# Kernel tuning notes

Measured on AMD Instinct MI355X. Metric: run time of the kernel, lower is better.

Reference implementation:

```python
import jax, jax.numpy as jnp
import numpy as np
from jax import lax
import math

N_QUBITS = 10
N_LAYERS = 4
PI = jnp.float32(math.pi)


def _c(x):
    return x.astype(jnp.complex64)


def rx_mat(t):
    c = _c(jnp.cos(0.5 * t)); s = _c(jnp.sin(0.5 * t))
    return jnp.stack([jnp.stack([c, -1j * s]), jnp.stack([-1j * s, c])])


def ry_mat(t):
    c = _c(jnp.cos(0.5 * t)); s = _c(jnp.sin(0.5 * t))
    return jnp.stack([jnp.stack([c, -s]), jnp.stack([s, c])])


def rz_mat(t):
    e0 = jnp.exp(_c(jnp.zeros_like(t)) - 0.5j * _c(t))
    e1 = jnp.exp(0.5j * _c(t))
    z = jnp.zeros_like(e0)
    return jnp.stack([jnp.stack([e0, z]), jnp.stack([z, e1])])


def apply_1q(psi, U, q):
    # psi: (2,)*n complex, apply 2x2 U on axis q
    psi = jnp.moveaxis(psi, q, 0)
    psi = jnp.tensordot(U, psi, axes=(1, 0))
    return jnp.moveaxis(psi, 0, q)


def apply_cnot(psi, ctrl, tgt):
    psi = jnp.moveaxis(psi, (ctrl, tgt), (0, 1))
    a00, a01, a10, a11 = psi[0, 0], psi[0, 1], psi[1, 0], psi[1, 1]
    psi = jnp.stack([jnp.stack([a00, a01]), jnp.stack([a11, a10])])
    return jnp.moveaxis(psi, (0, 1), (ctrl, tgt))


def vqc(state, weights):
    # state: (D,) float32 angles; weights: (layers, n, 3)
    n, L = N_QUBITS, N_LAYERS
    D = state.shape[0]
    psi = jnp.full((2,) * n, 2.0 ** (-n / 2.0), dtype=jnp.complex64)  # H^n |0>
    for layer in range(L):
        for q in range(n):
            ang = state[(layer * n + q) % D]
            psi = apply_1q(psi, rx_mat(ang), q)
            psi = apply_1q(psi, ry_mat(ang), q)
            psi = apply_1q(psi, rz_mat(weights[layer, q, 0]), q)
            psi = apply_1q(psi, ry_mat(weights[layer, q, 1]), q)
            psi = apply_1q(psi, rz_mat(weights[layer, q, 2]), q)
        for q in range(n - 1):
            psi = apply_cnot(psi, q, q + 1)
        psi = apply_cnot(psi, n - 1, 0)
    probs = jnp.real(psi * jnp.conj(psi))  # (2,)*n
    zdiag = jnp.array([1.0, -1.0], dtype=jnp.float32)
    exps = [jnp.sum(probs * zdiag.reshape((1,) * q + (2,) + (1,) * (n - q - 1)))
            for q in range(n)]
    return jnp.stack(exps)  # (n,)


def lstm_forward(x, W_ih, W_hh, b_ih, b_hh):
    # x: [B,T,Din]; PyTorch gate order: i, f, g, o
    B, T, _ = x.shape
    H = W_hh.shape[1]
    b = b_ih + b_hh

    def step(carry, xt):
        h, c = carry
        gates = xt @ W_ih.T + h @ W_hh.T + b
        i, f, g, o = jnp.split(gates, 4, axis=-1)
        i = jax.nn.sigmoid(i); f = jax.nn.sigmoid(f)
        g = jnp.tanh(g); o = jax.nn.sigmoid(o)
        c = f * c + i * g
        h = o * jnp.tanh(c)
        return (h, c), h

    h0 = jnp.zeros((B, H), x.dtype)
    c0 = jnp.zeros((B, H), x.dtype)
    _, hs = lax.scan(step, (h0, c0), jnp.swapaxes(x, 0, 1))
    return jnp.swapaxes(hs, 0, 1)  # [B,T,H]


def _forward(s, lstm_s, W_ih, W_hh, b_ih, b_hh, proj_W, proj_b,
             in_proj_W, in_proj_b, out_proj_W, out_proj_b,
             qweights, W1, b1, W2, b2):
    hs = lstm_forward(lstm_s, W_ih, W_hh, b_ih, b_hh)      # [B,T,H]
    lstm_last = hs[:, -1, :]                               # [B,H]
    state_full = jnp.concatenate([lstm_last, s], axis=1)   # [B,E]
    lstm_proj = hs @ proj_W.T + proj_b                     # [B,T,E]
    E = proj_W.shape[0]
    Wq, Wk, Wv = in_proj_W[:E], in_proj_W[E:2 * E], in_proj_W[2 * E:]
    bq, bk, bv = in_proj_b[:E], in_proj_b[E:2 * E], in_proj_b[2 * E:]
    q = state_full @ Wq.T + bq                             # [B,E] (1 query token)
    k = lstm_proj @ Wk.T + bk                              # [B,T,E]
    v = lstm_proj @ Wv.T + bv
    scale = 1.0 / jnp.sqrt(jnp.float32(E))                 # num_heads=1 -> head_dim=E
    attn = jax.nn.softmax(jnp.einsum('be,bte->bt', q, k) * scale, axis=-1)
    ctx = jnp.einsum('bt,bte->be', attn, v)
    attn_out = ctx @ out_proj_W.T + out_proj_b             # [B,E]
    merged_state = jnp.concatenate([attn_out, s], axis=1)  # [B,E+F]
    state_norm = jnp.tanh(merged_state) * PI
    qfeat = jax.vmap(lambda st: vqc(st, qweights))(state_norm)  # [B,n]
    merged = jnp.concatenate([merged_state, qfeat], axis=1)
    x = jax.nn.relu(merged @ W1.T + b1)
    return x @ W2.T + b2


def setup_inputs() -> dict:
    key = jax.random.key(0)
    ks = jax.random.split(key, 16)
    B, T = 512, 256
    Din, H, F = 128, 256, 64
    E = H + F          # 320 = state_dim
    Dm = E + F         # 384 = merged_state dim
    n_l1, n_act = 512, 8

    def g(k, shape, std):
        return (std * jax.random.normal(k, shape)).astype(jnp.float32)

    return {
        's': jax.random.normal(ks[0], (B, F), jnp.float32),
        'lstm_s': jax.random.normal(ks[1], (B, T, Din), jnp.float32),
        'W_ih': g(ks[2], (4 * H, Din), 0.05),
        'W_hh': g(ks[3], (4 * H, H), 0.05),
        'b_ih': jnp.zeros((4 * H,), jnp.float32),
        'b_hh': jnp.zeros((4 * H,), jnp.float32),
        'proj_W': g(ks[4], (E, H), 0.05),
        'proj_b': 0.1 * jnp.ones((E,), jnp.float32),
        'in_proj_W': g(ks[5], (3 * E, E), 0.05),
        'in_proj_b': jnp.zeros((3 * E,), jnp.float32),
        'out_proj_W': g(ks[6], (E, E), 0.05),
        'out_proj_b': jnp.zeros((E,), jnp.float32),
        'qweights': jax.random.uniform(ks[7], (N_LAYERS, N_QUBITS, 3), jnp.float32, 0.0, 2.0 * math.pi),
        'W1': g(ks[8], (n_l1, Dm + N_QUBITS), 0.05),
        'b1': 0.1 * jnp.ones((n_l1,), jnp.float32),
        'W2': g(ks[9], (n_act, n_l1), 0.05),
        'b2': 0.1 * jnp.ones((n_act,), jnp.float32),
    }


def reference(s, lstm_s, W_ih, W_hh, b_ih, b_hh, proj_W, proj_b,
              in_proj_W, in_proj_b, out_proj_W, out_proj_b,
              qweights, W1, b1, W2, b2):
    return _forward(s, lstm_s, W_ih, W_hh, b_ih, b_hh, proj_W, proj_b,
                    in_proj_W, in_proj_b, out_proj_W, out_proj_b,
                    qweights, W1, b1, W2, b2)
```

## Files before the change

kernel.cpp:

```cpp
#include <hip/hip_runtime.h>
#include <hip/hip_bf16.h>
#include <math.h>

typedef unsigned int u32;
typedef unsigned long long u64;
typedef unsigned short u16;
typedef __attribute__((ext_vector_type(8))) short short8;
typedef __attribute__((ext_vector_type(4))) float f32x4;
typedef __attribute__((ext_vector_type(4))) int v4i;

#define PI_F 3.14159265358979f
#define B_   512
#define T_   256
#define DIN  128
#define H_   256
#define G4   1024
#define F_   64
#define E_   320
#define DM   384
#define NL1  512
#define NACT 8
#define KMLP 394

__device__ v4i llvm_amdgcn_raw_buffer_load_v4i32(v4i rsrc, int voffset,
                                                 int soffset, int aux)
    __asm("llvm.amdgcn.raw.buffer.load.v4i32");
__device__ float llvm_amdgcn_raw_buffer_load_f32(v4i rsrc, int voffset,
                                                 int soffset, int aux)
    __asm("llvm.amdgcn.raw.buffer.load.f32");
__device__ void llvm_amdgcn_raw_buffer_store_i32(int vdata, v4i rsrc,
                                                 int voffset, int soffset,
                                                 int aux)
    __asm("llvm.amdgcn.raw.buffer.store.i32");
__device__ void llvm_amdgcn_raw_buffer_store_f32(float vdata, v4i rsrc,
                                                 int voffset, int soffset,
                                                 int aux)
    __asm("llvm.amdgcn.raw.buffer.store.f32");

__device__ __forceinline__ v4i make_srd(const void* p) {
  v4i r;
  r.x = (int)(u32)(u64)p;
  r.y = (int)(u32)((u64)p >> 32);
  r.z = (int)0xFFFFFFFFu;
  r.w = 0x00020000;
  return r;
}

__device__ __forceinline__ float b2f(u16 h) {
  union { u32 u; float f; } v; v.u = ((u32)h) << 16; return v.f;
}
__device__ __forceinline__ u16 f2b(float f) {
  union { float f; u32 u; } v; v.f = f;
  u32 r = (v.u + 0x7FFFu + ((v.u >> 16) & 1u)) >> 16;
  return (u16)r;
}
__device__ __forceinline__ float sigf(float x) { return 1.0f / (1.0f + __expf(-x)); }
__device__ __forceinline__ float tanhfast(float x) { return 2.0f / (1.0f + __expf(-2.0f * x)) - 1.0f; }
__device__ __forceinline__ float2 cmul(float2 a, float2 b) {
  return make_float2(a.x * b.x - a.y * b.y, a.x * b.y + a.y * b.x);
}
__device__ __forceinline__ float2 cadd(float2 a, float2 b) {
  return make_float2(a.x + b.x, a.y + b.y);
}

__global__ void k_prep1(const float* __restrict__ lstm_s,
                        const float* __restrict__ W_ih,
                        const float* __restrict__ W_hh,
                        const float* __restrict__ b_ih,
                        const float* __restrict__ b_hh,
                        const float* __restrict__ ipw,
                        const float* __restrict__ ipb,
                        const float* __restrict__ projb,
                        const float* __restrict__ qw,
                        const float* __restrict__ W1,
                        u16* __restrict__ xbf,
                        u16* __restrict__ hs,
                        u16* __restrict__ Wg,
                        float* __restrict__ bb,
                        float* __restrict__ W1t,
                        float* __restrict__ uw,
                        float* __restrict__ bkp,
                        float* __restrict__ bvp,
                        u32* __restrict__ cnt) {
  const int bid = blockIdx.x;
  const int tid = threadIdx.x;
  if (bid < 8192) {
    u32 u = (u32)bid * 256u + tid;
    u32 c8 = u & 15u, b = (u >> 4) & 511u, t = u >> 13;
    const float* src = lstm_s + ((size_t)b * T_ + t) * DIN + c8 * 8;
    union { u16 h[8]; uint4 v; } tmp;
#pragma unroll
    for (int i = 0; i < 8; ++i) tmp.h[i] = f2b(src[i]);
    *(uint4*)(xbf + ((size_t)t * B_ + b) * DIN + c8 * 8) = tmp.v;
  } else if (bid < 8384) {
    u32 u = (u32)(bid - 8192) * 256u + tid;
    u32 c8 = u % 48u, r = u / 48u;
    const float* src = (c8 < 16) ? (W_ih + (size_t)r * DIN + c8 * 8)
                                 : (W_hh + (size_t)r * H_ + (c8 - 16) * 8);
    union { u16 h[8]; uint4 v; } tmp;
#pragma unroll
    for (int i = 0; i < 8; ++i) tmp.h[i] = f2b(src[i]);
    *(uint4*)(Wg + (size_t)r * 384 + c8 * 8) = tmp.v;
  } else if (bid < 8448) {
    u32 u = (u32)(bid - 8384) * 256u + tid;
    ((uint4*)hs)[u] = make_uint4(0, 0, 0, 0);
  } else if (bid < 9236) {
    u32 u = (u32)(bid - 8448) * 256u + tid;
    u32 k = u / 512u, nn = u % 512u;
    W1t[u] = W1[(size_t)nn * KMLP + k];
  } else if (bid == 9236) {
    for (int i = tid; i < 1024; i += 256) bb[i] = b_ih[i] + b_hh[i];
    for (int i = tid; i < 1024; i += 256) cnt[i] = 0u;
    if (tid < 40) {
      float w0 = qw[tid * 3 + 0], w1 = qw[tid * 3 + 1], w2 = qw[tid * 3 + 2];
      float c0 = cosf(0.5f * w0), s0 = sinf(0.5f * w0);
      float c1 = cosf(0.5f * w1), s1 = sinf(0.5f * w1);
      float c2 = cosf(0.5f * w2), s2 = sinf(0.5f * w2);
      float2 e0m = make_float2(c0, -s0), e0p = make_float2(c0, s0);
      float2 e2m = make_float2(c2, -s2), e2p = make_float2(c2, s2);
      float2 t00 = make_float2(c1 * e0m.x, c1 * e0m.y);
      float2 t01 = make_float2(-s1 * e0p.x, -s1 * e0p.y);
      float2 t10 = make_float2(s1 * e0m.x, s1 * e0m.y);
      float2 t11 = make_float2(c1 * e0p.x, c1 * e0p.y);
      float2 u00 = cmul(e2m, t00), u01 = cmul(e2m, t01);
      float2 u10 = cmul(e2p, t10), u11 = cmul(e2p, t11);
      float* o = uw + tid * 8;
      o[0] = u00.x; o[1] = u00.y; o[2] = u01.x; o[3] = u01.y;
      o[4] = u10.x; o[5] = u10.y; o[6] = u11.x; o[7] = u11.y;
    }
  } else if (bid <= 9238) {
    int o = (bid - 9237) * 256 + tid;
    if (o < E_) {
      float acc = ipb[E_ + o];
      for (int e = 0; e < E_; ++e) acc += ipw[(size_t)(E_ + o) * E_ + e] * projb[e];
      bkp[o] = acc;
    }
  } else {
    int o = (bid - 9239) * 256 + tid;
    if (o < E_) {
      float acc = ipb[2 * E_ + o];
      for (int e = 0; e < E_; ++e) acc += ipw[(size_t)(2 * E_ + o) * E_ + e] * projb[e];
      bvp[o] = acc;
    }
  }
}

struct LstmArgs {
  const u16* xbf; u16* hs; const u16* Wg; const float* bb; u32* cnt;
  const float* ipw; const float* ipb; const float* projW;
  const float* opw; const float* opb;
  const float* bkp; const float* bvp;
  float* Wkp; float* Wvp;
  float* WuT; float* bu; float* wd; float* ddp; float* Wovt; float* bov;
};

__launch_bounds__(256, 1)
__global__ void k_lstm(LstmArgs A) {
  const int tid = threadIdx.x;
  __shared__ __align__(16) u16 Wl[32 * 392];

  if (blockIdx.x >= 256) {
    const int p = blockIdx.x - 256;
    const v4i kp_srd = make_srd(A.Wkp);
    const v4i vp_srd = make_srd(A.Wvp);
    float* lds_f = (float*)Wl;
    for (int o = p; o < E_; o += 256) {
      const float* rk = A.ipw + (size_t)(E_ + o) * E_;
      const float* rv = A.ipw + (size_t)(2 * E_ + o) * E_;
      float ak = 0.f, av = 0.f;
#pragma unroll 4
      for (int e = 0; e < E_; ++e) {
        float pw = A.projW[(size_t)e * H_ + tid];
        ak += rk[e] * pw;
        av += rv[e] * pw;
      }
      llvm_amdgcn_raw_buffer_store_f32(ak, kp_srd, (o * H_ + tid) * 4, 0, 17);
      llvm_amdgcn_raw_buffer_store_f32(av, vp_srd, (o * H_ + tid) * 4, 0, 17);
    }
    __syncthreads();
    if (tid == 0) {
      u32* pc = A.cnt + 768;
      __hip_atomic_fetch_add(pc, 1u, __ATOMIC_RELAXED, __HIP_MEMORY_SCOPE_AGENT);
      int guard = 0;
      while (__hip_atomic_load(pc, __ATOMIC_RELAXED, __HIP_MEMORY_SCOPE_AGENT) < 256u) {
        __builtin_amdgcn_s_sleep(1);
        if (++guard > (1 << 24)) break;
      }
    }
    __syncthreads();
    const int e0 = p, e1 = p + 256;
    for (int o = tid; o < E_; o += 256) {
      lds_f[o]      = A.ipw[(size_t)o * E_ + e0];
      lds_f[E_ + o] = (e1 < E_) ? A.ipw[(size_t)o * E_ + e1] : 0.f;
    }
    __syncthreads();
    {
      float a0 = 0.f, a1 = 0.f;
#pragma unroll 8
      for (int o = 0; o < E_; ++o) {
        float kv = llvm_amdgcn_raw_buffer_load_f32(kp_srd, (o * H_ + tid) * 4, 0, 17);
        a0 += kv * lds_f[o];
        a1 += kv * lds_f[E_ + o];
      }
      A.WuT[(size_t)e0 * H_ + tid] = a0;
      if (e1 < E_) A.WuT[(size_t)e1 * H_ + tid] = a1;
    }
    for (int o = tid; o < E_; o += 256)
      lds_f[2 * E_ + o] = llvm_amdgcn_raw_buffer_load_f32(vp_srd, (o * H_ + p) * 4, 0, 17);
    __syncthreads();
    {
      const int jj = p;
      for (int i = tid; i < E_; i += 256) {
        const float* wo = A.opw + (size_t)i * E_;
        float acc = 0.f;
#pragma unroll 8
        for (int o = 0; o < E_; ++o) acc += wo[o] * lds_f[2 * E_ + o];
        A.Wovt[(size_t)jj * E_ + i] = acc;
      }
    }
    if (p == 0) {
      {
        float acc = 0.f;
#pragma unroll 4
        for (int o = 0; o < E_; ++o) {
          float kv = llvm_amdgcn_raw_buffer_load_f32(kp_srd, (o * H_ + tid) * 4, 0, 17);
          acc += kv * A.ipb[o];
        }
        A.bu[tid] = acc;
      }
      for (int idx = tid; idx < E_; idx += 256) {
        float a1 = 0.f, a2 = A.opb[idx];
#pragma unroll 4
        for (int o = 0; o < E_; ++o) {
          a1 += A.ipw[(size_t)o * E_ + idx] * A.bkp[o];
          a2 += A.opw[(size_t)idx * E_ + o] * A.bvp[o];
        }
        A.wd[idx] = a1; A.bov[idx] = a2;
      }
      if (tid == 0) {
        float acc = 0.f;
        for (int o = 0; o < E_; ++o) acc += A.ipb[o] * A.bkp[o];
        A.ddp[0] = acc;
      }
    }
    return;
  }

  __builtin_amdgcn_s_setprio(1);
  const int g   = blockIdx.x & 7;
  const int n   = blockIdx.x >> 3;
  const int wid = tid >> 6, lane = tid & 63;

  for (int idx = tid; idx < 32 * 48; idx += 256) {
    int ln = idx / 48, c8 = idx % 48;
    int gr = (ln >> 3) * 256 + n * 8 + (ln & 7);
    *(uint4*)&Wl[ln * 392 + c8 * 8] = *(const uint4*)&A.Wg[(size_t)gr * 384 + c8 * 8];
  }
  const int j  = lane & 7;
  const int gc = n * 8 + j;
  const float bbi = A.bb[gc], bbf2 = A.bb[256 + gc];
  const float bbg = A.bb[512 + gc], bbo = A.bb[768 + gc];

  const int quad = lane >> 4;
  const int mrow = lane & 15;
  const int brow = g * 64 + wid * 16 + mrow;
  const int erow0 = g * 64 + wid * 16 + quad * 4;
  const bool hi = (lane & 8) != 0;
  float crs[4] = {0.f, 0.f, 0.f, 0.f};
  u32* mycnt = A.cnt + g * 64;
  u32 target = 0;

  const v4i hs_srd = make_srd(A.hs);
  const int hvoff = (brow * H_ + quad * 8) * 2;

  uint4 xc0, xc1, xc2, xc3, xn0, xn1, xn2, xn3;
  {
    const u16* xb = A.xbf + ((size_t)0 * B_ + brow) * DIN + quad * 8;
    xc0 = *(const uint4*)(xb + 0);
    xc1 = *(const uint4*)(xb + 32);
    xc2 = *(const uint4*)(xb + 64);
    xc3 = *(const uint4*)(xb + 96);
  }
  __syncthreads();

  for (int t = 0; t < T_; ++t) {
    const int hsoff = t * (B_ * H_ * 2);
    uint4 h0 = __builtin_bit_cast(uint4, llvm_amdgcn_raw_buffer_load_v4i32(hs_srd, hvoff +   0, hsoff, 17));
    uint4 h1 = __builtin_bit_cast(uint4, llvm_amdgcn_raw_buffer_load_v4i32(hs_srd, hvoff +  64, hsoff, 17));
    uint4 h2 = __builtin_bit_cast(uint4, llvm_amdgcn_raw_buffer_load_v4i32(hs_srd, hvoff + 128, hsoff, 17));
    uint4 h3 = __builtin_bit_cast(uint4, llvm_amdgcn_raw_buffer_load_v4i32(hs_srd, hvoff + 192, hsoff, 17));
    uint4 h4 = __builtin_bit_cast(uint4, llvm_amdgcn_raw_buffer_load_v4i32(hs_srd, hvoff + 256, hsoff, 17));
    uint4 h5 = __builtin_bit_cast(uint4, llvm_amdgcn_raw_buffer_load_v4i32(hs_srd, hvoff + 320, hsoff, 17));
    uint4 h6 = __builtin_bit_cast(uint4, llvm_amdgcn_raw_buffer_load_v4i32(hs_srd, hvoff + 384, hsoff, 17));
    uint4 h7 = __builtin_bit_cast(uint4, llvm_amdgcn_raw_buffer_load_v4i32(hs_srd, hvoff + 448, hsoff, 17));
    {
      const int tn = (t + 1 < T_) ? (t + 1) : t;
      const u16* xb = A.xbf + ((size_t)tn * B_ + brow) * DIN + quad * 8;
      xn0 = *(const uint4*)(xb + 0);
      xn1 = *(const uint4*)(xb + 32);
      xn2 = *(const uint4*)(xb + 64);
      xn3 = *(const uint4*)(xb + 96);
    }

    f32x4 acc0 = {0.f, 0.f, 0.f, 0.f}, acc1 = {0.f, 0.f, 0.f, 0.f};
#define MMSTEP(AV, KOFF)                                                          \
    {                                                                             \
      short8 av  = __builtin_bit_cast(short8, AV);                                \
      short8 bv0 = __builtin_bit_cast(short8,                                     \
          *(const uint4*)&Wl[mrow * 392 + (KOFF) + quad * 8]);                    \
      short8 bv1 = __builtin_bit_cast(short8,                                     \
          *(const uint4*)&Wl[(16 + mrow) * 392 + (KOFF) + quad * 8]);             \
      acc0 = __builtin_amdgcn_mfma_f32_16x16x32_bf16(av, bv0, acc0, 0, 0, 0);     \
      acc1 = __builtin_amdgcn_mfma_f32_16x16x32_bf16(av, bv1, acc1, 0, 0, 0);     \
    }
    MMSTEP(xc0, 0)   MMSTEP(xc1, 32)  MMSTEP(xc2, 64)  MMSTEP(xc3, 96)
    MMSTEP(h0, 128)  MMSTEP(h1, 160)  MMSTEP(h2, 192)  MMSTEP(h3, 224)
    MMSTEP(h4, 256)  MMSTEP(h5, 288)  MMSTEP(h6, 320)  MMSTEP(h7, 352)
#undef MMSTEP

    const int hsoff_o = (t + 1) * (B_ * H_ * 2);
#pragma unroll
    for (int r = 0; r < 4; ++r) {
      float x0 = acc0[r], x1v = acc1[r];
      float y0 = __shfl_xor(x0, 8, 64);
      float y1 = __shfl_xor(x1v, 8, 64);
      float iv = (hi ? y0 : x0) + bbi;
      float fv = (hi ? x0 : y0) + bbf2;
      float gv = (hi ? y1 : x1v) + bbg;
      float ov = (hi ? x1v : y1) + bbo;
      float cc = sigf(fv) * crs[r] + sigf(iv) * tanhfast(gv);
      crs[r] = cc;
      float hh = sigf(ov) * tanhfast(cc);
      float hh2 = __shfl_xor(hh, 1, 64);
      if (!hi && ((j & 1) == 0)) {
        u32 pk = (u32)f2b(hh) | ((u32)f2b(hh2) << 16);
        llvm_amdgcn_raw_buffer_store_i32((int)pk, hs_srd,
                                         ((erow0 + r) * H_ + gc) * 2, hsoff_o, 17);
      }
    }
    target += 32;
    if (t != T_ - 1) {
      __syncthreads();
      if (tid == 0) {
        __hip_atomic_fetch_add(mycnt, 1u, __ATOMIC_RELAXED, __HIP_MEMORY_SCOPE_AGENT);
        int guard = 0;
        while (__hip_atomic_load(mycnt, __ATOMIC_RELAXED, __HIP_MEMORY_SCOPE_AGENT) < target) {
          __builtin_amdgcn_s_sleep(1);
          if (++guard > (1 << 24)) break;
        }
      }
      __syncthreads();
      xc0 = xn0; xc1 = xn1; xc2 = xn2; xc3 = xn3;
    }
  }
}

__global__ void k_post(const u16* __restrict__ hs, const float* __restrict__ s,
                       const float* __restrict__ WuT, const float* __restrict__ bu,
                       const float* __restrict__ wd, const float* __restrict__ ddp,
                       const float* __restrict__ Wovt, const float* __restrict__ bov,
                       const float* __restrict__ uwg,
                       const float* __restrict__ W1t, const float* __restrict__ b1,
                       const float* __restrict__ W2, const float* __restrict__ b2,
                       float* __restrict__ out) {
  int b = blockIdx.x, tid = threadIdx.x;
  int wid = tid >> 6, lane = tid & 63;
  __shared__ float z[E_];
  __shared__ float red[256];
  __shared__ float ul_s[H_];
  __shared__ float sc[T_];
  __shared__ float wv_s[H_];
  __shared__ float mst_l[DM];
  __shared__ float dvec_s;
  __shared__ float2 psi[1024];
  __shared__ float ang[40];
  __shared__ float uwl[320];
  __shared__ float part[4][10];
  __shared__ float qf_s[10];
  __shared__ float mg[KMLP];
  __shared__ float x1[NL1];

  z[tid] = b2f(hs[((size_t)T_ * B_ + b) * H_ + tid]);
  if (tid < F_) z[H_ + tid] = s[(size_t)b * F_ + tid];
  __syncthreads();
  {
    float a0 = bu[tid], a1 = 0.f;
#pragma unroll 8
    for (int e = 0; e < 160; ++e) {
      a0 += WuT[(size_t)e * H_ + tid] * z[e];
      a1 += WuT[(size_t)(e + 160) * H_ + tid] * z[e + 160];
    }
    ul_s[tid] = a0 + a1;
    float p = 0.f;
    for (int e = tid; e < E_; e += 256) p += wd[e] * z[e];
    red[tid] = p;
    __syncthreads();
    for (int s2 = 128; s2 > 0; s2 >>= 1) {
      if (tid < s2) red[tid] += red[tid + s2];
      __syncthreads();
    }
    if (tid == 0) dvec_s = red[0] + ddp[0];
    __syncthreads();
  }

  {
    const float db = dvec_s;
    const float scale = 0.055901699437494745f;
    float4 ul = make_float4(ul_s[lane * 4], ul_s[lane * 4 + 1],
                            ul_s[lane * 4 + 2], ul_s[lane * 4 + 3]);
    for (int tt = 0; tt < 64; ++tt) {
      int t = wid * 64 + tt;
      u32 rw0 = ((const u32*)(hs + ((size_t)(t + 1) * B_ + b) * H_))[lane * 2];
      u32 rw1 = ((const u32*)(hs + ((size_t)(t + 1) * B_ + b) * H_))[lane * 2 + 1];
      union { u32 uu; float f; } f0, f1, f2, f3;
      f0.uu = rw0 << 16; f1.uu = rw0 & 0xFFFF0000u;
      f2.uu = rw1 << 16; f3.uu = rw1 & 0xFFFF0000u;
      float p = f0.f * ul.x + f1.f * ul.y + f2.f * ul.z + f3.f * ul.w;
#pragma unroll
      for (int off = 32; off > 0; off >>= 1) p += __shfl_xor(p, off, 64);
      if (lane == 0) sc[t] = (p + db) * scale;
    }
    __syncthreads();
    float v = sc[tid];
    red[tid] = v;
    __syncthreads();
    for (int s2 = 128; s2 > 0; s2 >>= 1) {
      if (tid < s2) red[tid] = fmaxf(red[tid], red[tid + s2]);
      __syncthreads();
    }
    float m = red[0];
    __syncthreads();
    float e = __expf(v - m);
    red[tid] = e;
    __syncthreads();
    for (int s2 = 128; s2 > 0; s2 >>= 1) {
      if (tid < s2) red[tid] += red[tid + s2];
      __syncthreads();
    }
    float inv = 1.f / red[0];
    __syncthreads();
    sc[tid] = e * inv;
    __syncthreads();
    float a0 = 0.f, a1 = 0.f;
#pragma unroll 8
    for (int t = 0; t < 128; ++t) {
      a0 += sc[t]       * b2f(hs[((size_t)(t + 1) * B_ + b) * H_ + tid]);
      a1 += sc[t + 128] * b2f(hs[((size_t)(t + 129) * B_ + b) * H_ + tid]);
    }
    wv_s[tid] = a0 + a1;
    __syncthreads();
  }

  {
    for (int i = tid; i < E_; i += 256) {
      float a0 = bov[i], a1 = 0.f;
#pragma unroll 8
      for (int jj = 0; jj < 128; ++jj) {
        a0 += Wovt[(size_t)jj * E_ + i] * wv_s[jj];
        a1 += Wovt[(size_t)(jj + 128) * E_ + i] * wv_s[jj + 128];
      }
      mst_l[i] = a0 + a1;
    }
    if (tid < F_) mst_l[E_ + tid] = s[(size_t)b * F_ + tid];
    __syncthreads();
  }

  {
    if (tid < 40) ang[tid] = tanhf(mst_l[tid]) * PI_F;
    uwl[tid] = uwg[tid];
    if (tid < 64) uwl[256 + tid] = uwg[256 + tid];
#pragma unroll
    for (int k = 0; k < 4; ++k) psi[tid + k * 256] = make_float2(0.03125f, 0.f);
    __syncthreads();
    for (int l = 0; l < 4; ++l) {
      for (int q = 0; q < 10; ++q) {
        int lq = l * 10 + q;
        float a = ang[lq];
        float ca = __cosf(0.5f * a), sa = __sinf(0.5f * a);
        float cs = ca * sa;
        float2 m00 = make_float2(ca * ca, sa * sa);
        float2 m01 = make_float2(-cs, -cs);
        float2 m10 = make_float2(cs, -cs);
        float2 m11 = make_float2(ca * ca, -sa * sa);
        const float* uwp = &uwl[lq * 8];
        float2 a00 = make_float2(uwp[0], uwp[1]), a01 = make_float2(uwp[2], uwp[3]);
        float2 a10 = make_float2(uwp[4], uwp[5]), a11 = make_float2(uwp[6], uwp[7]);
        float2 u00 = cadd(cmul(a00, m00), cmul(a01, m10));
        float2 u01 = cadd(cmul(a00, m01), cmul(a01, m11));
        float2 u10 = cadd(cmul(a10, m00), cmul(a11, m10));
        float2 u11 = cadd(cmul(a10, m01), cmul(a11, m11));
        int bp = 9 - q;
        __syncthreads();
#pragma unroll
        for (int k = 0; k < 2; ++k) {
          int p = tid + k * 256;
          int i0 = ((p >> bp) << (bp + 1)) | (p & ((1 << bp) - 1));
          int i1 = i0 | (1 << bp);
          float2 A0 = psi[i0], A1 = psi[i1];
          psi[i0] = cadd(cmul(u00, A0), cmul(u01, A1));
          psi[i1] = cadd(cmul(u10, A0), cmul(u11, A1));
        }
      }
      for (int q = 0; q < 9; ++q) {
        int lo = 8 - q;
        __syncthreads();
        int p = tid;
        int i0 = ((p >> lo) << (lo + 2)) | (2 << lo) | (p & ((1 << lo) - 1));
        int i1 = i0 | (1 << lo);
        float2 tmp = psi[i0]; psi[i0] = psi[i1]; psi[i1] = tmp;
      }
      __syncthreads();
      {
        int i0 = (tid << 1) | 1;
        int i1 = i0 | 512;
        float2 tmp = psi[i0]; psi[i0] = psi[i1]; psi[i1] = tmp;
      }
    }
    __syncthreads();
    float acc[10];
#pragma unroll
    for (int q = 0; q < 10; ++q) acc[q] = 0.f;
#pragma unroll
    for (int k = 0; k < 4; ++k) {
      int idx = tid + k * 256;
      float2 A = psi[idx];
      float pr = A.x * A.x + A.y * A.y;
#pragma unroll
      for (int q = 0; q < 10; ++q) acc[q] += ((idx >> (9 - q)) & 1) ? -pr : pr;
    }
#pragma unroll
    for (int q = 0; q < 10; ++q) {
      float vq = acc[q];
#pragma unroll
      for (int off = 32; off > 0; off >>= 1) vq += __shfl_xor(vq, off, 64);
      if (lane == 0) part[wid][q] = vq;
    }
    __syncthreads();
    if (tid < 10) qf_s[tid] = part[0][tid] + part[1][tid] + part[2][tid] + part[3][tid];
  }

  {
    for (int i = tid; i < DM; i += 256) mg[i] = mst_l[i];
    if (tid < 10) mg[DM + tid] = qf_s[tid];
    __syncthreads();
    float a0 = b1[tid], a1 = b1[tid + 256];
#pragma unroll 8
    for (int k = 0; k < KMLP; ++k) {
      float m = mg[k];
      a0 += W1t[(size_t)k * NL1 + tid] * m;
      a1 += W1t[(size_t)k * NL1 + tid + 256] * m;
    }
    x1[tid] = fmaxf(a0, 0.f);
    x1[tid + 256] = fmaxf(a1, 0.f);
    __syncthreads();
    int a = tid >> 5, l32 = tid & 31;
    float p = 0.f;
    for (int k = l32; k < NL1; k += 32) p += x1[k] * W2[(size_t)a * NL1 + k];
    red[tid] = p;
    __syncthreads();
    if (tid < 8) {
      float acc = b2[tid];
#pragma unroll
      for (int i = 0; i < 32; ++i) acc += red[tid * 32 + i];
      out[(size_t)b * NACT + tid] = acc;
    }
  }
}

extern "C" void kernel_launch(void* const* d_in, const int* in_sizes, int n_in,
                              void* d_out, int out_size, void* d_ws, size_t ws_size,
                              hipStream_t stream) {
  const float* s      = (const float*)d_in[0];
  const float* lstm_s = (const float*)d_in[1];
  const float* W_ih   = (const float*)d_in[2];
  const float* W_hh   = (const float*)d_in[3];
  const float* b_ih   = (const float*)d_in[4];
  const float* b_hh   = (const float*)d_in[5];
  const float* projW  = (const float*)d_in[6];
  const float* projb  = (const float*)d_in[7];
  const float* ipw    = (const float*)d_in[8];
  const float* ipb    = (const float*)d_in[9];
  const float* opw    = (const float*)d_in[10];
  const float* opb    = (const float*)d_in[11];
  const float* qw     = (const float*)d_in[12];
  const float* W1     = (const float*)d_in[13];
  const float* b1     = (const float*)d_in[14];
  const float* W2     = (const float*)d_in[15];
  const float* b2     = (const float*)d_in[16];
  float* out = (float*)d_out;

  char* wsb = (char*)d_ws;
  size_t off = 0;
  auto alloc = [&](size_t bytes) -> void* {
    void* p = wsb + off;
    off = (off + bytes + 255) & ~(size_t)255;
    return p;
  };
  u16*  xbf  = (u16*)alloc((size_t)T_ * B_ * DIN * 2);
  u16*  hs   = (u16*)alloc((size_t)(T_ + 1) * B_ * H_ * 2);
  u16*  Wg   = (u16*)alloc((size_t)G4 * 384 * 2);
  float* bb  = (float*)alloc(G4 * 4);
  float* Wkp = (float*)alloc((size_t)E_ * H_ * 4);
  float* Wvp = (float*)alloc((size_t)E_ * H_ * 4);
  float* bkp = (float*)alloc(E_ * 4);
  float* bvp = (float*)alloc(E_ * 4);
  float* WuT = (float*)alloc((size_t)E_ * H_ * 4);
  float* bu  = (float*)alloc(H_ * 4);
  float* wd  = (float*)alloc(E_ * 4);
  float* ddp = (float*)alloc(256);
  float* Wovt= (float*)alloc((size_t)H_ * E_ * 4);
  float* bov = (float*)alloc(E_ * 4);
  float* uw  = (float*)alloc(40 * 8 * 4);
  float* W1t = (float*)alloc((size_t)KMLP * NL1 * 4);
  u32*  cnt  = (u32*)alloc(1024 * 4);
  (void)ws_size; (void)in_sizes; (void)n_in; (void)out_size;

  hipLaunchKernelGGL(k_prep1, dim3(9241), dim3(256), 0, stream,
                     lstm_s, W_ih, W_hh, b_ih, b_hh, ipw, ipb, projb, qw, W1,
                     xbf, hs, Wg, bb, W1t, uw, bkp, bvp, cnt);

  LstmArgs la;
  la.xbf = xbf; la.hs = hs; la.Wg = Wg; la.bb = bb; la.cnt = cnt;
  la.ipw = ipw; la.ipb = ipb; la.projW = projW; la.opw = opw; la.opb = opb;
  la.bkp = bkp; la.bvp = bvp; la.Wkp = Wkp; la.Wvp = Wvp;
  la.WuT = WuT; la.bu = bu; la.wd = wd; la.ddp = ddp; la.Wovt = Wovt; la.bov = bov;
  void* kargs[] = { (void*)&la };
  hipError_t ce = hipLaunchCooperativeKernel(reinterpret_cast<const void*>(&k_lstm),
                                             dim3(512), dim3(256), kargs, 0, stream);
  if (ce != hipSuccess) {
    hipLaunchKernelGGL(k_lstm, dim3(512), dim3(256), 0, stream, la);
  }

  hipLaunchKernelGGL(k_post, dim3(512), dim3(256), 0, stream,
                     hs, s, WuT, bu, wd, ddp, Wovt, bov, uw, W1t, b1, W2, b2, out);
}
```

Measured before the change: 1.184 ms.

## Reassociate attention weight products to drop cross-block barrier; move W1 transpose into LSTM side blocks

```diff
diff --git a/kernel.cpp b/kernel.cpp
--- a/kernel.cpp
+++ b/kernel.cpp
@@ -25,17 +25,10 @@
 __device__ v4i llvm_amdgcn_raw_buffer_load_v4i32(v4i rsrc, int voffset,
                                                  int soffset, int aux)
     __asm("llvm.amdgcn.raw.buffer.load.v4i32");
-__device__ float llvm_amdgcn_raw_buffer_load_f32(v4i rsrc, int voffset,
-                                                 int soffset, int aux)
-    __asm("llvm.amdgcn.raw.buffer.load.f32");
 __device__ void llvm_amdgcn_raw_buffer_store_i32(int vdata, v4i rsrc,
                                                  int voffset, int soffset,
                                                  int aux)
     __asm("llvm.amdgcn.raw.buffer.store.i32");
-__device__ void llvm_amdgcn_raw_buffer_store_f32(float vdata, v4i rsrc,
-                                                 int voffset, int soffset,
-                                                 int aux)
-    __asm("llvm.amdgcn.raw.buffer.store.f32");
 
 __device__ __forceinline__ v4i make_srd(const void* p) {
   v4i r;
@@ -72,12 +65,10 @@
                         const float* __restrict__ ipb,
                         const float* __restrict__ projb,
                         const float* __restrict__ qw,
-                        const float* __restrict__ W1,
                         u16* __restrict__ xbf,
                         u16* __restrict__ hs,
                         u16* __restrict__ Wg,
                         float* __restrict__ bb,
-                        float* __restrict__ W1t,
                         float* __restrict__ uw,
                         float* __restrict__ bkp,
                         float* __restrict__ bvp,
@@ -104,11 +95,7 @@
   } else if (bid < 8448) {
     u32 u = (u32)(bid - 8384) * 256u + tid;
     ((uint4*)hs)[u] = make_uint4(0, 0, 0, 0);
-  } else if (bid < 9236) {
-    u32 u = (u32)(bid - 8448) * 256u + tid;
-    u32 k = u / 512u, nn = u % 512u;
-    W1t[u] = W1[(size_t)nn * KMLP + k];
-  } else if (bid == 9236) {
+  } else if (bid == 8448) {
     for (int i = tid; i < 1024; i += 256) bb[i] = b_ih[i] + b_hh[i];
     for (int i = tid; i < 1024; i += 256) cnt[i] = 0u;
     if (tid < 40) {
@@ -128,15 +115,15 @@
       o[0] = u00.x; o[1] = u00.y; o[2] = u01.x; o[3] = u01.y;
       o[4] = u10.x; o[5] = u10.y; o[6] = u11.x; o[7] = u11.y;
     }
-  } else if (bid <= 9238) {
-    int o = (bid - 9237) * 256 + tid;
+  } else if (bid <= 8450) {
+    int o = (bid - 8449) * 256 + tid;
     if (o < E_) {
       float acc = ipb[E_ + o];
       for (int e = 0; e < E_; ++e) acc += ipw[(size_t)(E_ + o) * E_ + e] * projb[e];
       bkp[o] = acc;
     }
   } else {
-    int o = (bid - 9239) * 256 + tid;
+    int o = (bid - 8451) * 256 + tid;
     if (o < E_) {
       float acc = ipb[2 * E_ + o];
       for (int e = 0; e < E_; ++e) acc += ipw[(size_t)(2 * E_ + o) * E_ + e] * projb[e];
@@ -150,7 +137,7 @@
   const float* ipw; const float* ipb; const float* projW;
   const float* opw; const float* opb;
   const float* bkp; const float* bvp;
-  float* Wkp; float* Wvp;
+  const float* W1; float* W1t;
   float* WuT; float* bu; float* wd; float* ddp; float* Wovt; float* bov;
 };
 
@@ -161,72 +148,75 @@
 
   if (blockIdx.x >= 256) {
     const int p = blockIdx.x - 256;
-    const v4i kp_srd = make_srd(A.Wkp);
-    const v4i vp_srd = make_srd(A.Wvp);
     float* lds_f = (float*)Wl;
-    for (int o = p; o < E_; o += 256) {
-      const float* rk = A.ipw + (size_t)(E_ + o) * E_;
-      const float* rv = A.ipw + (size_t)(2 * E_ + o) * E_;
-      float ak = 0.f, av = 0.f;
-#pragma unroll 4
-      for (int e = 0; e < E_; ++e) {
-        float pw = A.projW[(size_t)e * H_ + tid];
-        ak += rk[e] * pw;
-        av += rv[e] * pw;
-      }
-      llvm_amdgcn_raw_buffer_store_f32(ak, kp_srd, (o * H_ + tid) * 4, 0, 17);
-      llvm_amdgcn_raw_buffer_store_f32(av, vp_srd, (o * H_ + tid) * 4, 0, 17);
-    }
-    __syncthreads();
-    if (tid == 0) {
-      u32* pc = A.cnt + 768;
-      __hip_atomic_fetch_add(pc, 1u, __ATOMIC_RELAXED, __HIP_MEMORY_SCOPE_AGENT);
-      int guard = 0;
-      while (__hip_atomic_load(pc, __ATOMIC_RELAXED, __HIP_MEMORY_SCOPE_AGENT) < 256u) {
-        __builtin_amdgcn_s_sleep(1);
-        if (++guard > (1 << 24)) break;
-      }
-    }
-    __syncthreads();
-    const int e0 = p, e1 = p + 256;
-    for (int o = tid; o < E_; o += 256) {
-      lds_f[o]      = A.ipw[(size_t)o * E_ + e0];
-      lds_f[E_ + o] = (e1 < E_) ? A.ipw[(size_t)o * E_ + e1] : 0.f;
-    }
-    __syncthreads();
-    {
-      float a0 = 0.f, a1 = 0.f;
-#pragma unroll 8
-      for (int o = 0; o < E_; ++o) {
-        float kv = llvm_amdgcn_raw_buffer_load_f32(kp_srd, (o * H_ + tid) * 4, 0, 17);
-        a0 += kv * lds_f[o];
-        a1 += kv * lds_f[E_ + o];
-      }
-      A.WuT[(size_t)e0 * H_ + tid] = a0;
-      if (e1 < E_) A.WuT[(size_t)e1 * H_ + tid] = a1;
-    }
-    for (int o = tid; o < E_; o += 256)
-      lds_f[2 * E_ + o] = llvm_amdgcn_raw_buffer_load_f32(vp_srd, (o * H_ + p) * 4, 0, 17);
-    __syncthreads();
-    {
-      const int jj = p;
-      for (int i = tid; i < E_; i += 256) {
-        const float* wo = A.opw + (size_t)i * E_;
-        float acc = 0.f;
-#pragma unroll 8
-        for (int o = 0; o < E_; ++o) acc += wo[o] * lds_f[2 * E_ + o];
-        A.Wovt[(size_t)jj * E_ + i] = acc;
-      }
-    }
+
+    for (u32 u = (u32)p * 256u + tid; u < (u32)KMLP * NL1; u += 65536u) {
+      u32 k = u / 512u, nn = u % 512u;
+      A.W1t[u] = A.W1[(size_t)nn * KMLP + k];
+    }
+
+    for (int e = p; e < E_; e += 256) {
+      for (int e2 = tid; e2 < E_; e2 += 256) {
+        float m0 = 0.f, m1 = 0.f;
+#pragma unroll 8
+        for (int o = 0; o < E_; o += 2) {
+          m0 += A.ipw[(size_t)o * E_ + e]       * A.ipw[(size_t)(E_ + o) * E_ + e2];
+          m1 += A.ipw[(size_t)(o + 1) * E_ + e] * A.ipw[(size_t)(E_ + o + 1) * E_ + e2];
+        }
+        lds_f[e2] = m0 + m1;
+      }
+      __syncthreads();
+      {
+        float a0 = 0.f, a1 = 0.f;
+#pragma unroll 8
+        for (int e2 = 0; e2 < E_; e2 += 2) {
+          a0 += lds_f[e2]     * A.projW[(size_t)e2 * H_ + tid];
+          a1 += lds_f[e2 + 1] * A.projW[(size_t)(e2 + 1) * H_ + tid];
+        }
+        A.WuT[(size_t)e * H_ + tid] = a0 + a1;
+      }
+      __syncthreads();
+    }
+
+    for (int i = p; i < E_; i += 256) {
+      const float* wo = A.opw + (size_t)i * E_;
+      for (int e2 = tid; e2 < E_; e2 += 256) {
+        float m0 = 0.f, m1 = 0.f;
+#pragma unroll 8
+        for (int o = 0; o < E_; o += 2) {
+          m0 += wo[o]     * A.ipw[(size_t)(2 * E_ + o) * E_ + e2];
+          m1 += wo[o + 1] * A.ipw[(size_t)(2 * E_ + o + 1) * E_ + e2];
+        }
+        lds_f[e2] = m0 + m1;
+      }
+      __syncthreads();
+      {
+        float a0 = 0.f, a1 = 0.f;
+#pragma unroll 8
+        for (int e2 = 0; e2 < E_; e2 += 2) {
+          a0 += lds_f[e2]     * A.projW[(size_t)e2 * H_ + tid];
+          a1 += lds_f[e2 + 1] * A.projW[(size_t)(e2 + 1) * H_ + tid];
+        }
+        A.Wovt[(size_t)tid * E_ + i] = a0 + a1;
+      }
+      __syncthreads();
+    }
+
     if (p == 0) {
-      {
+      for (int e2 = tid; e2 < E_; e2 += 256) {
         float acc = 0.f;
 #pragma unroll 4
-        for (int o = 0; o < E_; ++o) {
-          float kv = llvm_amdgcn_raw_buffer_load_f32(kp_srd, (o * H_ + tid) * 4, 0, 17);
-          acc += kv * A.ipb[o];
-        }
-        A.bu[tid] = acc;
+        for (int o = 0; o < E_; ++o)
+          acc += A.ipb[o] * A.ipw[(size_t)(E_ + o) * E_ + e2];
+        lds_f[e2] = acc;
+      }
+      __syncthreads();
+      {
+        float a0 = 0.f;
+#pragma unroll 4
+        for (int e2 = 0; e2 < E_; ++e2)
+          a0 += lds_f[e2] * A.projW[(size_t)e2 * H_ + tid];
+        A.bu[tid] = a0;
       }
       for (int idx = tid; idx < E_; idx += 256) {
         float a1 = 0.f, a2 = A.opb[idx];
@@ -600,8 +590,6 @@
   u16*  hs   = (u16*)alloc((size_t)(T_ + 1) * B_ * H_ * 2);
   u16*  Wg   = (u16*)alloc((size_t)G4 * 384 * 2);
   float* bb  = (float*)alloc(G4 * 4);
-  float* Wkp = (float*)alloc((size_t)E_ * H_ * 4);
-  float* Wvp = (float*)alloc((size_t)E_ * H_ * 4);
   float* bkp = (float*)alloc(E_ * 4);
   float* bvp = (float*)alloc(E_ * 4);
   float* WuT = (float*)alloc((size_t)E_ * H_ * 4);
@@ -615,14 +603,14 @@
   u32*  cnt  = (u32*)alloc(1024 * 4);
   (void)ws_size; (void)in_sizes; (void)n_in; (void)out_size;
 
-  hipLaunchKernelGGL(k_prep1, dim3(9241), dim3(256), 0, stream,
-                     lstm_s, W_ih, W_hh, b_ih, b_hh, ipw, ipb, projb, qw, W1,
-                     xbf, hs, Wg, bb, W1t, uw, bkp, bvp, cnt);
+  hipLaunchKernelGGL(k_prep1, dim3(8453), dim3(256), 0, stream,
+                     lstm_s, W_ih, W_hh, b_ih, b_hh, ipw, ipb, projb, qw,
+                     xbf, hs, Wg, bb, uw, bkp, bvp, cnt);
 
   LstmArgs la;
   la.xbf = xbf; la.hs = hs; la.Wg = Wg; la.bb = bb; la.cnt = cnt;
   la.ipw = ipw; la.ipb = ipb; la.projW = projW; la.opw = opw; la.opb = opb;
-  la.bkp = bkp; la.bvp = bvp; la.Wkp = Wkp; la.Wvp = Wvp;
+  la.bkp = bkp; la.bvp = bvp; la.W1 = W1; la.W1t = W1t;
   la.WuT = WuT; la.bu = bu; la.wd = wd; la.ddp = ddp; la.Wovt = Wovt; la.bov = bov;
   void* kargs[] = { (void*)&la };
   hipError_t ce = hipLaunchCooperativeKernel(reinterpret_cast<const void*>(&k_lstm),
```

Result: no change. 1.176 ms (-0.6%).
